# Kernel optimization log

Hardware: AMD Instinct MI355X
Metric: run time of the kernel (lower is better)

## Reference

```python
import jax, jax.numpy as jnp
import numpy as np

B, S, D, F, E, K = 4, 4096, 1024, 2048, 8, 2


def setup_inputs() -> dict:
    key = jax.random.key(0)
    ks = jax.random.split(key, 5)
    s = lambda n: 1.0 / np.sqrt(n).astype(np.float32)
    return {
        "hidden_states": jax.random.normal(ks[0], (B, S, D), jnp.float32),
        "router_w": jax.random.normal(ks[1], (E, D), jnp.float32) * s(D),
        "w_gate": jax.random.normal(ks[2], (E, F, D), jnp.float32) * s(D),
        "w_up": jax.random.normal(ks[3], (E, F, D), jnp.float32) * s(D),
        "w_down": jax.random.normal(ks[4], (E, D, F), jnp.float32) * s(F),
    }


def reference(hidden_states, router_w, w_gate, w_up, w_down):
    b, s, d = hidden_states.shape
    e = router_w.shape[0]
    x = hidden_states.reshape(-1, d)  # [T, D], T = B*S

    # --- router: softmax over expert logits, top-k, renormalize (norm_topk_prob) ---
    logits = x @ router_w.T                                   # [T, E]
    scores = jax.nn.softmax(logits.astype(jnp.float32), axis=-1)
    topk_w, topk_idx = jax.lax.top_k(scores, K)               # [T, K]
    topk_w = topk_w / jnp.sum(topk_w, axis=-1, keepdims=True)

    # dense per-(token, expert) combine weight: sum of topk weights routed to e
    cw = jnp.sum(jax.nn.one_hot(topk_idx, e, dtype=topk_w.dtype)
                 * topk_w[..., None], axis=1)                 # [T, E]
    cw = cw.astype(x.dtype)

    # --- experts: SwiGLU MLP per expert, weighted-combined; scan keeps memory low ---
    def per_expert(acc, wts):
        wg, wu, wd, cwe = wts                                  # [F,D],[F,D],[D,F],[T]
        h = jax.nn.silu(x @ wg.T) * (x @ wu.T)                 # [T, F]
        return acc + cwe[:, None] * (h @ wd.T), None

    out, _ = jax.lax.scan(per_expert, jnp.zeros_like(x),
                          (w_gate, w_up, w_down, cw.T))
    return out.reshape(b, s, d)
```

## Files before the change

### kernel.cpp

```cpp
#include <hip/hip_runtime.h>
#include <stdint.h>

#define T_TOK 16384
#define DDIM  1024
#define FDIM  2048
#define NEXP  8
#define MAX_SLOTS 33792
#define NMT (MAX_SLOTS / 128)

typedef __attribute__((ext_vector_type(8))) short bf16x8;
typedef __attribute__((ext_vector_type(4))) float f32x4;

typedef __attribute__((address_space(1))) void gvoid_t;
typedef __attribute__((address_space(3))) void lvoid_t;

#define META_CNT 0
#define META_CUR 256
#define META_OFF 512
#define META_MEXP 544

__device__ __forceinline__ void cp16(void* lds, const void* g) {
  __builtin_amdgcn_global_load_lds((gvoid_t*)g, (lvoid_t*)lds, 16, 0, 0);
}

__device__ __forceinline__ unsigned short f2bf(float f) {
  union { float f; unsigned int u; } v; v.f = f;
  unsigned int u = v.u;
  return (unsigned short)((u + 0x7fffu + ((u >> 16) & 1u)) >> 16);
}

__device__ __forceinline__ int xcd_remap(int bid, int nwg) {
  int xcd = bid & 7, i = bid >> 3;
  int q = nwg >> 3, r = nwg & 7;
  int base = (xcd < r) ? xcd * (q + 1) : r * (q + 1) + (xcd - r) * q;
  return base + i;
}

__global__ void router_kernel(const float* __restrict__ x, const float* __restrict__ rw,
                              int* __restrict__ tk_idx, float* __restrict__ tk_w,
                              unsigned short* __restrict__ xb) {
  const int wid = threadIdx.x >> 6;
  const int lane = threadIdx.x & 63;
  const int t = blockIdx.x * 4 + wid;
  const float4* xr = (const float4*)(x + (size_t)t * DDIM);
  float4 xv[4];
#pragma unroll
  for (int i = 0; i < 4; i++) xv[i] = xr[lane + 64 * i];
  ushort4* xbr = (ushort4*)(xb + (size_t)t * DDIM);
#pragma unroll
  for (int i = 0; i < 4; i++) {
    ushort4 o;
    o.x = f2bf(xv[i].x); o.y = f2bf(xv[i].y); o.z = f2bf(xv[i].z); o.w = f2bf(xv[i].w);
    xbr[lane + 64 * i] = o;
  }
  float lg[NEXP];
#pragma unroll
  for (int e = 0; e < NEXP; e++) {
    const float4* we = (const float4*)(rw + e * DDIM);
    float s = 0.f;
#pragma unroll
    for (int i = 0; i < 4; i++) {
      float4 v = we[lane + 64 * i];
      s += xv[i].x * v.x + xv[i].y * v.y + xv[i].z * v.z + xv[i].w * v.w;
    }
#pragma unroll
    for (int m = 32; m > 0; m >>= 1) s += __shfl_xor(s, m, 64);
    lg[e] = s;
  }
  int i0 = 0; float m0 = lg[0];
#pragma unroll
  for (int e = 1; e < NEXP; e++) if (lg[e] > m0) { m0 = lg[e]; i0 = e; }
  int i1 = -1; float m1 = -3.0e38f;
#pragma unroll
  for (int e = 0; e < NEXP; e++) if (e != i0 && lg[e] > m1) { m1 = lg[e]; i1 = e; }
  if (lane == 0) {
    float ee = __expf(m1 - m0);
    float w0 = 1.f / (1.f + ee);
    tk_idx[2 * t] = i0; tk_idx[2 * t + 1] = i1;
    tk_w[2 * t] = w0;  tk_w[2 * t + 1] = ee / (1.f + ee);
  }
}

__global__ void hist_kernel(const int* __restrict__ tk_idx, int* __restrict__ meta) {
  int* counts_p = meta + META_CNT;
  int t = blockIdx.x * 256 + threadIdx.x;
  int w = threadIdx.x >> 6, lane = threadIdx.x & 63;
  int e0 = tk_idx[2 * t], e1 = tk_idx[2 * t + 1];
  __shared__ int cnt[4][NEXP];
#pragma unroll
  for (int e = 0; e < NEXP; e++) {
    unsigned long long m0 = __ballot(e0 == e), m1 = __ballot(e1 == e);
    if (lane == 0) cnt[w][e] = __popcll(m0) + __popcll(m1);
  }
  __syncthreads();
  if (threadIdx.x < NEXP) {
    int e = threadIdx.x;
    atomicAdd(&counts_p[e * 32], cnt[0][e] + cnt[1][e] + cnt[2][e] + cnt[3][e]);
  }
}

__global__ void scan_kernel(int* __restrict__ meta) {
  int* counts_p = meta + META_CNT;
  int* offp     = meta + META_OFF;
  int* mexp     = meta + META_MEXP;
  __shared__ int soff[NEXP + 1];
  if (threadIdx.x == 0) {
    int acc = 0;
    for (int e = 0; e < NEXP; e++) {
      offp[e] = acc; soff[e] = acc;
      acc += (counts_p[e * 32] + 127) & ~127;
    }
    offp[NEXP] = acc; soff[NEXP] = acc;
  }
  __syncthreads();
  for (int m = threadIdx.x; m < NMT; m += blockDim.x) {
    int s = m * 128;
    int e = -1;
#pragma unroll
    for (int q = 0; q < NEXP; q++)
      if (s >= soff[q] && s < soff[q + 1]) { e = q; break; }
    mexp[m] = e;
  }
}

__global__ void scatter_kernel(const int* __restrict__ tk_idx, const float* __restrict__ tk_w,
                               int* __restrict__ meta,
                               int* __restrict__ slot_token, float* __restrict__ slot_w) {
  const int* offp = meta + META_OFF;
  int* cursors_p  = meta + META_CUR;
  int t = blockIdx.x * 256 + threadIdx.x;
  int w = threadIdx.x >> 6, lane = threadIdx.x & 63;
  int e0 = tk_idx[2 * t], e1 = tk_idx[2 * t + 1];
  unsigned long long lmask = (1ull << lane) - 1ull;
  __shared__ int cnt[4][NEXP], woff[4][NEXP], base[NEXP];
  int r0 = 0, r1 = 0;
#pragma unroll
  for (int e = 0; e < NEXP; e++) {
    unsigned long long m0 = __ballot(e0 == e), m1 = __ballot(e1 == e);
    int c0 = __popcll(m0);
    if (lane == 0) cnt[w][e] = c0 + __popcll(m1);
    if (e0 == e) r0 = __popcll(m0 & lmask);
    if (e1 == e) r1 = c0 + __popcll(m1 & lmask);
  }
  __syncthreads();
  if (threadIdx.x < NEXP) {
    int e = threadIdx.x, acc = 0;
#pragma unroll
    for (int ww = 0; ww < 4; ww++) { woff[ww][e] = acc; acc += cnt[ww][e]; }
    base[e] = atomicAdd(&cursors_p[e * 32], acc);
  }
  __syncthreads();
  int p0 = offp[e0] + base[e0] + woff[w][e0] + r0;
  int p1 = offp[e1] + base[e1] + woff[w][e1] + r1;
  slot_token[p0] = t; slot_w[p0] = tk_w[2 * t];
  slot_token[p1] = t; slot_w[p1] = tk_w[2 * t + 1];
}

#define W4EACH (1 << 22)
__global__ void cvt3_kernel(const float* __restrict__ wg, const float* __restrict__ wu,
                            const float* __restrict__ wd,
                            unsigned short* __restrict__ wgb, unsigned short* __restrict__ wub,
                            unsigned short* __restrict__ wdb) {
  int i = blockIdx.x * blockDim.x + threadIdx.x;
  int stride = gridDim.x * blockDim.x;
  for (; i < 3 * W4EACH; i += stride) {
    int which = i >> 22, j = i & (W4EACH - 1);
    const float4* s = (const float4*)(which == 0 ? wg : which == 1 ? wu : wd);
    ushort4* d = (ushort4*)(which == 0 ? wgb : which == 1 ? wub : wdb);
    float4 v = s[j];
    ushort4 o;
    o.x = f2bf(v.x); o.y = f2bf(v.y); o.z = f2bf(v.z); o.w = f2bf(v.w);
    d[j] = o;
  }
}

__global__ __launch_bounds__(256)
void gemm1_kernel(const unsigned short* __restrict__ xb,
                  const unsigned short* __restrict__ wgb,
                  const unsigned short* __restrict__ wub,
                  const int* __restrict__ meta,
                  const int* __restrict__ slot_token,
                  unsigned short* __restrict__ h, int m0) {
  const int wgid = xcd_remap((int)blockIdx.x, (int)gridDim.x);
  const int gm = m0 + (wgid >> 5);
  const int e = meta[META_MEXP + gm];
  if (e < 0) return;
  const int n0 = (wgid & 31) * 64;

  __shared__ alignas(16) unsigned short As[128 * 64];
  __shared__ alignas(16) unsigned short Bgs[64 * 64];
  __shared__ alignas(16) unsigned short Bus[64 * 64];

  const int tid = threadIdx.x;
  const int wid = tid >> 6;
  const int lane = tid & 63;
  const int wr = wid >> 1, wc = wid & 1;

  const unsigned int slog = (unsigned int)(((lane & 7) ^ (lane >> 3)) << 4);
  const char* const xbB = (const char*)xb;
  const char* const wgB = (const char*)wgb + ((size_t)e * FDIM + n0) * (DDIM * 2);
  const char* const wuB = (const char*)wub + ((size_t)e * FDIM + n0) * (DDIM * 2);

  const char* asrc[4]; unsigned int aldc[4];
#pragma unroll
  for (int q = 0; q < 4; q++) {
    int chunk = q * 4 + wid;
    int row = chunk * 8 + (lane >> 3);
    int tok = slot_token[gm * 128 + row];
    tok = tok < 0 ? 0 : tok;
    asrc[q] = xbB + (size_t)tok * (DDIM * 2) + slog;
    aldc[q] = chunk * 1024;
  }
  const char* bgsrc[2]; const char* busrc[2]; unsigned int bldc[2];
#pragma unroll
  for (int q = 0; q < 2; q++) {
    int chunk = q * 4 + wid;
    int row = chunk * 8 + (lane >> 3);
    bgsrc[q] = wgB + (size_t)row * (DDIM * 2) + slog;
    busrc[q] = wuB + (size_t)row * (DDIM * 2) + slog;
    bldc[q] = chunk * 1024;
  }

  const int lr = lane & 15, lk = lane >> 4;
  const unsigned int fsw = (unsigned int)((lane & 7) << 4);
  unsigned int aoff[4][2], boff[2][2];
#pragma unroll
  for (int mf = 0; mf < 4; mf++)
#pragma unroll
    for (int kc = 0; kc < 2; kc++) {
      unsigned int lg = (unsigned int)(kc * 64 + lk * 16);
      aoff[mf][kc] = (unsigned int)(wr * 64 + mf * 16 + lr) * 128 + (lg ^ fsw);
    }
#pragma unroll
  for (int nf = 0; nf < 2; nf++)
#pragma unroll
    for (int kc = 0; kc < 2; kc++) {
      unsigned int lg = (unsigned int)(kc * 64 + lk * 16);
      boff[nf][kc] = (unsigned int)(wc * 32 + nf * 16 + lr) * 128 + (lg ^ fsw);
    }

  f32x4 accg[4][2] = {};
  f32x4 accu[4][2] = {};
  const char* asb = (const char*)As;
  const char* bgsb = (const char*)Bgs;
  const char* busb = (const char*)Bus;

  for (int kt = 0; kt < DDIM / 64; kt++) {
    const int koff = kt * 128;
#pragma unroll
    for (int q = 0; q < 2; q++) {
      cp16((char*)Bgs + bldc[q], bgsrc[q] + koff);
      cp16((char*)Bus + bldc[q], busrc[q] + koff);
    }
#pragma unroll
    for (int q = 0; q < 4; q++) cp16((char*)As + aldc[q], asrc[q] + koff);
    __syncthreads();
#pragma unroll
    for (int kc = 0; kc < 2; kc++) {
      bf16x8 af[4], bgf[2], buf2[2];
#pragma unroll
      for (int mf = 0; mf < 4; mf++) af[mf] = *(const bf16x8*)(asb + aoff[mf][kc]);
#pragma unroll
      for (int nf = 0; nf < 2; nf++) {
        bgf[nf] = *(const bf16x8*)(bgsb + boff[nf][kc]);
        buf2[nf] = *(const bf16x8*)(busb + boff[nf][kc]);
      }
#pragma unroll
      for (int mf = 0; mf < 4; mf++)
#pragma unroll
        for (int nf = 0; nf < 2; nf++) {
          accg[mf][nf] = __builtin_amdgcn_mfma_f32_16x16x32_bf16(af[mf], bgf[nf], accg[mf][nf], 0, 0, 0);
          accu[mf][nf] = __builtin_amdgcn_mfma_f32_16x16x32_bf16(af[mf], buf2[nf], accu[mf][nf], 0, 0, 0);
        }
    }
    __syncthreads();
  }

  unsigned short* hB = h + (size_t)(gm - m0) * 128 * FDIM;
#pragma unroll
  for (int mf = 0; mf < 4; mf++)
#pragma unroll
    for (int nf = 0; nf < 2; nf++) {
      f32x4 g = accg[mf][nf], u = accu[mf][nf];
#pragma unroll
      for (int j = 0; j < 4; j++) {
        float gv = g[j];
        float hv = (gv / (1.f + __expf(-gv))) * u[j];
        int row = wr * 64 + mf * 16 + lk * 4 + j;
        int col = n0 + wc * 32 + nf * 16 + lr;
        hB[(size_t)row * FDIM + col] = f2bf(hv);
      }
    }
}

__global__ __launch_bounds__(256)
void gemm2_kernel(const unsigned short* __restrict__ h,
                  const unsigned short* __restrict__ wdb,
                  const int* __restrict__ meta,
                  const int* __restrict__ slot_token,
                  const float* __restrict__ slot_w,
                  float* __restrict__ out, int m0) {
  const int wgid = xcd_remap((int)blockIdx.x, (int)gridDim.x);
  const int gm = m0 + (wgid >> 3);
  const int e = meta[META_MEXP + gm];
  if (e < 0) return;
  const int n0 = (wgid & 7) * 128;

  __shared__ alignas(16) unsigned short As[128 * 64];
  __shared__ alignas(16) unsigned short Bs[128 * 64];

  const int tid = threadIdx.x;
  const int wid = tid >> 6;
  const int lane = tid & 63;
  const int wr = wid >> 1, wc = wid & 1;

  const unsigned int slog = (unsigned int)(((lane & 7) ^ (lane >> 3)) << 4);
  const char* const hB = (const char*)h + (size_t)(gm - m0) * 128 * (FDIM * 2);
  const char* const wdB = (const char*)wdb + ((size_t)e * DDIM + n0) * (FDIM * 2);

  const char* asrc[4]; const char* bsrc[4]; unsigned int ldc[4];
#pragma unroll
  for (int q = 0; q < 4; q++) {
    int chunk = q * 4 + wid;
    int row = chunk * 8 + (lane >> 3);
    asrc[q] = hB + (size_t)row * (FDIM * 2) + slog;
    bsrc[q] = wdB + (size_t)row * (FDIM * 2) + slog;
    ldc[q] = chunk * 1024;
  }

  const int lr = lane & 15, lk = lane >> 4;
  const unsigned int fsw = (unsigned int)((lane & 7) << 4);
  unsigned int aoff[4][2], boff[4][2];
#pragma unroll
  for (int f = 0; f < 4; f++)
#pragma unroll
    for (int kc = 0; kc < 2; kc++) {
      unsigned int lg = (unsigned int)(kc * 64 + lk * 16);
      aoff[f][kc] = (unsigned int)(wr * 64 + f * 16 + lr) * 128 + (lg ^ fsw);
      boff[f][kc] = (unsigned int)(wc * 64 + f * 16 + lr) * 128 + (lg ^ fsw);
    }

  f32x4 acc[4][4] = {};
  const char* asb = (const char*)As;
  const char* bsb = (const char*)Bs;

  for (int kt = 0; kt < FDIM / 64; kt++) {
    const int koff = kt * 128;
#pragma unroll
    for (int q = 0; q < 4; q++) {
      cp16((char*)As + ldc[q], asrc[q] + koff);
      cp16((char*)Bs + ldc[q], bsrc[q] + koff);
    }
    __syncthreads();
#pragma unroll
    for (int kc = 0; kc < 2; kc++) {
      bf16x8 af[4], bff[4];
#pragma unroll
      for (int mf = 0; mf < 4; mf++) af[mf] = *(const bf16x8*)(asb + aoff[mf][kc]);
#pragma unroll
      for (int nf = 0; nf < 4; nf++) bff[nf] = *(const bf16x8*)(bsb + boff[nf][kc]);
#pragma unroll
      for (int mf = 0; mf < 4; mf++)
#pragma unroll
        for (int nf = 0; nf < 4; nf++)
          acc[mf][nf] = __builtin_amdgcn_mfma_f32_16x16x32_bf16(af[mf], bff[nf], acc[mf][nf], 0, 0, 0);
    }
    __syncthreads();
  }

#pragma unroll
  for (int mf = 0; mf < 4; mf++)
#pragma unroll
    for (int j = 0; j < 4; j++) {
      int slot = gm * 128 + wr * 64 + mf * 16 + lk * 4 + j;
      int tok = slot_token[slot];
      if (tok < 0) continue;
      float w = slot_w[slot];
      float* orow = out + (size_t)tok * DDIM + n0 + wc * 64 + lr;
#pragma unroll
      for (int nf = 0; nf < 4; nf++)
        atomicAdd(orow + nf * 16, w * acc[mf][nf][j]);
    }
}

static constexpr size_t WB       = (size_t)NEXP * FDIM * DDIM * 2;
static constexpr size_t OFF_WG   = 0;
static constexpr size_t OFF_WU   = OFF_WG + WB;
static constexpr size_t OFF_WD   = OFF_WU + WB;
static constexpr size_t OFF_XB   = OFF_WD + WB;
static constexpr size_t XBB      = (size_t)T_TOK * DDIM * 2;
static constexpr size_t OFF_ST   = OFF_XB + XBB;
static constexpr size_t OFF_SW   = OFF_ST + (size_t)MAX_SLOTS * 4;
static constexpr size_t OFF_TI   = OFF_SW + (size_t)MAX_SLOTS * 4;
static constexpr size_t OFF_TW   = OFF_TI + (size_t)T_TOK * 2 * 4;
static constexpr size_t OFF_META = OFF_TW + (size_t)T_TOK * 2 * 4;
static constexpr size_t OFF_H    = OFF_ST + 1048576;
static constexpr size_t MT_BYTES = (size_t)128 * FDIM * 2;

extern "C" void kernel_launch(void* const* d_in, const int* in_sizes, int n_in,
                              void* d_out, int out_size, void* d_ws, size_t ws_size,
                              hipStream_t stream) {
  const float* x  = (const float*)d_in[0];
  const float* rw = (const float*)d_in[1];
  const float* wg = (const float*)d_in[2];
  const float* wu = (const float*)d_in[3];
  const float* wd = (const float*)d_in[4];
  float* out = (float*)d_out;

  char* ws = (char*)d_ws;
  unsigned short* wgb = (unsigned short*)(ws + OFF_WG);
  unsigned short* wub = (unsigned short*)(ws + OFF_WU);
  unsigned short* wdb = (unsigned short*)(ws + OFF_WD);
  unsigned short* xb  = (unsigned short*)(ws + OFF_XB);
  unsigned short* h   = (unsigned short*)(ws + OFF_H);
  int*   slot_token = (int*)(ws + OFF_ST);
  float* slot_w     = (float*)(ws + OFF_SW);
  int*   tk_idx     = (int*)(ws + OFF_TI);
  float* tk_w       = (float*)(ws + OFF_TW);
  int*   meta       = (int*)(ws + OFF_META);

  size_t avail = ws_size > OFF_H ? ws_size - OFF_H : 0;
  int wmt = (int)(avail / MT_BYTES);
  if (wmt > NMT) wmt = NMT;
  if (wmt < 8) wmt = 8;

  (void)hipMemsetAsync(out, 0, (size_t)out_size * sizeof(float), stream);
  (void)hipMemsetAsync(meta, 0, 2048, stream);
  (void)hipMemsetAsync(slot_token, 0xFF, (size_t)MAX_SLOTS * 4, stream);

  cvt3_kernel<<<4096, 256, 0, stream>>>(wg, wu, wd, wgb, wub, wdb);
  router_kernel<<<T_TOK / 4, 256, 0, stream>>>(x, rw, tk_idx, tk_w, xb);
  hist_kernel<<<T_TOK / 256, 256, 0, stream>>>(tk_idx, meta);
  scan_kernel<<<1, 256, 0, stream>>>(meta);
  scatter_kernel<<<T_TOK / 256, 256, 0, stream>>>(tk_idx, tk_w, meta, slot_token, slot_w);

  for (int m0 = 0; m0 < NMT; m0 += wmt) {
    int mc = (NMT - m0 < wmt) ? (NMT - m0) : wmt;
    gemm1_kernel<<<mc * 32, 256, 0, stream>>>(xb, wgb, wub, meta, slot_token, h, m0);
    gemm2_kernel<<<mc * 8, 256, 0, stream>>>(h, wdb, meta, slot_token, slot_w, out, m0);
  }
}
```

Measured before the change: 759.1 us.

## Pre-gather routed tokens into contiguous bf16 buffer and enlarge gemm1 N tile

Replaces the router's dense bf16 copy of x with a gather kernel that writes routed tokens into a slot-ordered contiguous bf16 buffer, so gemm1 reads A rows contiguously instead of indirecting through slot_token. Gemm1's N tile doubles from 64 to 128, giving each wave a 4x4 fragment grid so each A fragment is reused across more MFMAs, and the gate and up MFMAs are split into separate phases. It also drops the XCD-aware block remap in favour of a plain 2D grid. The costs are an extra gather pass over about 33K slots, higher register and LDS pressure that may lower occupancy, and possibly worse L2 locality across XCDs.

```diff
diff --git a/kernel.cpp b/kernel.cpp
--- a/kernel.cpp
+++ b/kernel.cpp
@@ -37,8 +37,7 @@
 }
 
 __global__ void router_kernel(const float* __restrict__ x, const float* __restrict__ rw,
-                              int* __restrict__ tk_idx, float* __restrict__ tk_w,
-                              unsigned short* __restrict__ xb) {
+                              int* __restrict__ tk_idx, float* __restrict__ tk_w) {
   const int wid = threadIdx.x >> 6;
   const int lane = threadIdx.x & 63;
   const int t = blockIdx.x * 4 + wid;
@@ -46,13 +45,6 @@
   float4 xv[4];
 #pragma unroll
   for (int i = 0; i < 4; i++) xv[i] = xr[lane + 64 * i];
-  ushort4* xbr = (ushort4*)(xb + (size_t)t * DDIM);
-#pragma unroll
-  for (int i = 0; i < 4; i++) {
-    ushort4 o;
-    o.x = f2bf(xv[i].x); o.y = f2bf(xv[i].y); o.z = f2bf(xv[i].z); o.w = f2bf(xv[i].w);
-    xbr[lane + 64 * i] = o;
-  }
   float lg[NEXP];
 #pragma unroll
   for (int e = 0; e < NEXP; e++) {
@@ -174,22 +166,35 @@
   }
 }
 
+__global__ void gather_kernel(const float* __restrict__ x, const int* __restrict__ slot_token,
+                              unsigned short* __restrict__ xg) {
+  int slot = blockIdx.x;
+  int t = slot_token[slot];
+  int c = threadIdx.x * 4;
+  ushort4 o;
+  if (t >= 0) {
+    float4 v = *(const float4*)(x + (size_t)t * DDIM + c);
+    o.x = f2bf(v.x); o.y = f2bf(v.y); o.z = f2bf(v.z); o.w = f2bf(v.w);
+  } else {
+    o.x = 0; o.y = 0; o.z = 0; o.w = 0;
+  }
+  *(ushort4*)(xg + (size_t)slot * DDIM + c) = o;
+}
+
 __global__ __launch_bounds__(256)
-void gemm1_kernel(const unsigned short* __restrict__ xb,
+void gemm1_kernel(const unsigned short* __restrict__ xg,
                   const unsigned short* __restrict__ wgb,
                   const unsigned short* __restrict__ wub,
                   const int* __restrict__ meta,
-                  const int* __restrict__ slot_token,
                   unsigned short* __restrict__ h, int m0) {
-  const int wgid = xcd_remap((int)blockIdx.x, (int)gridDim.x);
-  const int gm = m0 + (wgid >> 5);
+  const int gm = m0 + blockIdx.y;
   const int e = meta[META_MEXP + gm];
   if (e < 0) return;
-  const int n0 = (wgid & 31) * 64;
+  const int n0 = blockIdx.x * 128;
 
   __shared__ alignas(16) unsigned short As[128 * 64];
-  __shared__ alignas(16) unsigned short Bgs[64 * 64];
-  __shared__ alignas(16) unsigned short Bus[64 * 64];
+  __shared__ alignas(16) unsigned short Bgs[128 * 64];
+  __shared__ alignas(16) unsigned short Bus[128 * 64];
 
   const int tid = threadIdx.x;
   const int wid = tid >> 6;
@@ -197,50 +202,35 @@
   const int wr = wid >> 1, wc = wid & 1;
 
   const unsigned int slog = (unsigned int)(((lane & 7) ^ (lane >> 3)) << 4);
-  const char* const xbB = (const char*)xb;
+  const char* const xgB = (const char*)xg;
   const char* const wgB = (const char*)wgb + ((size_t)e * FDIM + n0) * (DDIM * 2);
   const char* const wuB = (const char*)wub + ((size_t)e * FDIM + n0) * (DDIM * 2);
 
-  const char* asrc[4]; unsigned int aldc[4];
+  const char* asrc[4]; const char* bgsrc[4]; const char* busrc[4]; unsigned int ldc[4];
 #pragma unroll
   for (int q = 0; q < 4; q++) {
     int chunk = q * 4 + wid;
     int row = chunk * 8 + (lane >> 3);
-    int tok = slot_token[gm * 128 + row];
-    tok = tok < 0 ? 0 : tok;
-    asrc[q] = xbB + (size_t)tok * (DDIM * 2) + slog;
-    aldc[q] = chunk * 1024;
-  }
-  const char* bgsrc[2]; const char* busrc[2]; unsigned int bldc[2];
-#pragma unroll
-  for (int q = 0; q < 2; q++) {
-    int chunk = q * 4 + wid;
-    int row = chunk * 8 + (lane >> 3);
+    asrc[q]  = xgB + (size_t)(gm * 128 + row) * (DDIM * 2) + slog;
     bgsrc[q] = wgB + (size_t)row * (DDIM * 2) + slog;
     busrc[q] = wuB + (size_t)row * (DDIM * 2) + slog;
-    bldc[q] = chunk * 1024;
+    ldc[q] = chunk * 1024;
   }
 
   const int lr = lane & 15, lk = lane >> 4;
   const unsigned int fsw = (unsigned int)((lane & 7) << 4);
-  unsigned int aoff[4][2], boff[2][2];
-#pragma unroll
-  for (int mf = 0; mf < 4; mf++)
+  unsigned int aoff[4][2], boff[4][2];
+#pragma unroll
+  for (int f = 0; f < 4; f++)
 #pragma unroll
     for (int kc = 0; kc < 2; kc++) {
       unsigned int lg = (unsigned int)(kc * 64 + lk * 16);
-      aoff[mf][kc] = (unsigned int)(wr * 64 + mf * 16 + lr) * 128 + (lg ^ fsw);
-    }
-#pragma unroll
-  for (int nf = 0; nf < 2; nf++)
-#pragma unroll
-    for (int kc = 0; kc < 2; kc++) {
-      unsigned int lg = (unsigned int)(kc * 64 + lk * 16);
-      boff[nf][kc] = (unsigned int)(wc * 32 + nf * 16 + lr) * 128 + (lg ^ fsw);
-    }
-
-  f32x4 accg[4][2] = {};
-  f32x4 accu[4][2] = {};
+      aoff[f][kc] = (unsigned int)(wr * 64 + f * 16 + lr) * 128 + (lg ^ fsw);
+      boff[f][kc] = (unsigned int)(wc * 64 + f * 16 + lr) * 128 + (lg ^ fsw);
+    }
+
+  f32x4 accg[4][4] = {};
+  f32x4 accu[4][4] = {};
   const char* asb = (const char*)As;
   const char* bgsb = (const char*)Bgs;
   const char* busb = (const char*)Bus;
@@ -248,30 +238,31 @@
   for (int kt = 0; kt < DDIM / 64; kt++) {
     const int koff = kt * 128;
 #pragma unroll
-    for (int q = 0; q < 2; q++) {
-      cp16((char*)Bgs + bldc[q], bgsrc[q] + koff);
-      cp16((char*)Bus + bldc[q], busrc[q] + koff);
-    }
-#pragma unroll
-    for (int q = 0; q < 4; q++) cp16((char*)As + aldc[q], asrc[q] + koff);
+    for (int q = 0; q < 4; q++) {
+      cp16((char*)As + ldc[q], asrc[q] + koff);
+      cp16((char*)Bgs + ldc[q], bgsrc[q] + koff);
+      cp16((char*)Bus + ldc[q], busrc[q] + koff);
+    }
     __syncthreads();
 #pragma unroll
     for (int kc = 0; kc < 2; kc++) {
-      bf16x8 af[4], bgf[2], buf2[2];
+      bf16x8 af[4], bgf[4], buf2[4];
 #pragma unroll
       for (int mf = 0; mf < 4; mf++) af[mf] = *(const bf16x8*)(asb + aoff[mf][kc]);
 #pragma unroll
-      for (int nf = 0; nf < 2; nf++) {
-        bgf[nf] = *(const bf16x8*)(bgsb + boff[nf][kc]);
-        buf2[nf] = *(const bf16x8*)(busb + boff[nf][kc]);
-      }
+      for (int nf = 0; nf < 4; nf++) bgf[nf] = *(const bf16x8*)(bgsb + boff[nf][kc]);
 #pragma unroll
       for (int mf = 0; mf < 4; mf++)
 #pragma unroll
-        for (int nf = 0; nf < 2; nf++) {
+        for (int nf = 0; nf < 4; nf++)
           accg[mf][nf] = __builtin_amdgcn_mfma_f32_16x16x32_bf16(af[mf], bgf[nf], accg[mf][nf], 0, 0, 0);
+#pragma unroll
+      for (int nf = 0; nf < 4; nf++) buf2[nf] = *(const bf16x8*)(busb + boff[nf][kc]);
+#pragma unroll
+      for (int mf = 0; mf < 4; mf++)
+#pragma unroll
+        for (int nf = 0; nf < 4; nf++)
           accu[mf][nf] = __builtin_amdgcn_mfma_f32_16x16x32_bf16(af[mf], buf2[nf], accu[mf][nf], 0, 0, 0);
-        }
     }
     __syncthreads();
   }
@@ -280,14 +271,14 @@
 #pragma unroll
   for (int mf = 0; mf < 4; mf++)
 #pragma unroll
-    for (int nf = 0; nf < 2; nf++) {
+    for (int nf = 0; nf < 4; nf++) {
       f32x4 g = accg[mf][nf], u = accu[mf][nf];
 #pragma unroll
       for (int j = 0; j < 4; j++) {
         float gv = g[j];
         float hv = (gv / (1.f + __expf(-gv))) * u[j];
         int row = wr * 64 + mf * 16 + lk * 4 + j;
-        int col = n0 + wc * 32 + nf * 16 + lr;
+        int col = n0 + wc * 64 + nf * 16 + lr;
         hB[(size_t)row * FDIM + col] = f2bf(hv);
       }
     }
@@ -387,9 +378,9 @@
 static constexpr size_t OFF_WG   = 0;
 static constexpr size_t OFF_WU   = OFF_WG + WB;
 static constexpr size_t OFF_WD   = OFF_WU + WB;
-static constexpr size_t OFF_XB   = OFF_WD + WB;
-static constexpr size_t XBB      = (size_t)T_TOK * DDIM * 2;
-static constexpr size_t OFF_ST   = OFF_XB + XBB;
+static constexpr size_t OFF_XG   = OFF_WD + WB;
+static constexpr size_t XGB      = (size_t)MAX_SLOTS * DDIM * 2;
+static constexpr size_t OFF_ST   = OFF_XG + XGB;
 static constexpr size_t OFF_SW   = OFF_ST + (size_t)MAX_SLOTS * 4;
 static constexpr size_t OFF_TI   = OFF_SW + (size_t)MAX_SLOTS * 4;
 static constexpr size_t OFF_TW   = OFF_TI + (size_t)T_TOK * 2 * 4;
@@ -411,7 +402,7 @@
   unsigned short* wgb = (unsigned short*)(ws + OFF_WG);
   unsigned short* wub = (unsigned short*)(ws + OFF_WU);
   unsigned short* wdb = (unsigned short*)(ws + OFF_WD);
-  unsigned short* xb  = (unsigned short*)(ws + OFF_XB);
+  unsigned short* xg  = (unsigned short*)(ws + OFF_XG);
   unsigned short* h   = (unsigned short*)(ws + OFF_H);
   int*   slot_token = (int*)(ws + OFF_ST);
   float* slot_w     = (float*)(ws + OFF_SW);
@@ -429,14 +420,15 @@
   (void)hipMemsetAsync(slot_token, 0xFF, (size_t)MAX_SLOTS * 4, stream);
 
   cvt3_kernel<<<4096, 256, 0, stream>>>(wg, wu, wd, wgb, wub, wdb);
-  router_kernel<<<T_TOK / 4, 256, 0, stream>>>(x, rw, tk_idx, tk_w, xb);
+  router_kernel<<<T_TOK / 4, 256, 0, stream>>>(x, rw, tk_idx, tk_w);
   hist_kernel<<<T_TOK / 256, 256, 0, stream>>>(tk_idx, meta);
   scan_kernel<<<1, 256, 0, stream>>>(meta);
   scatter_kernel<<<T_TOK / 256, 256, 0, stream>>>(tk_idx, tk_w, meta, slot_token, slot_w);
+  gather_kernel<<<MAX_SLOTS, 256, 0, stream>>>(x, slot_token, xg);
 
   for (int m0 = 0; m0 < NMT; m0 += wmt) {
     int mc = (NMT - m0 < wmt) ? (NMT - m0) : wmt;
-    gemm1_kernel<<<mc * 32, 256, 0, stream>>>(xb, wgb, wub, meta, slot_token, h, m0);
+    gemm1_kernel<<<dim3(FDIM / 128, mc), 256, 0, stream>>>(xg, wgb, wub, meta, h, m0);
     gemm2_kernel<<<mc * 8, 256, 0, stream>>>(h, wdb, meta, slot_token, slot_w, out, m0);
   }
 }
```

After: 1.025 ms. +35.0%, slower.

## Pre-gather routed token rows into contiguous buffer before gate/up GEMM

Applied to the files above, without the earlier changes.

Adds a gather kernel that copies each slot's bf16 token row into a dense per-slot buffer, so gemm1 loads A tiles from contiguous rows instead of indirecting through slot_token. It also drops the XCD-aware block remapping in favour of a 2D grid. The cost is an extra pass that writes about 69MB and a larger workspace, which shifts the start of h and shrinks the number of m-tiles per chunk. Losing the XCD remap may also reduce L2 reuse of the weights.

```diff
diff --git a/kernel.cpp b/kernel.cpp
--- a/kernel.cpp
+++ b/kernel.cpp
@@ -174,18 +174,28 @@
   }
 }
 
+__global__ void gather_kernel(const unsigned short* __restrict__ xb,
+                              const int* __restrict__ slot_token,
+                              unsigned short* __restrict__ xg) {
+  int slot = blockIdx.x;
+  int t = slot_token[slot];
+  int c = threadIdx.x * 4;
+  ushort4 o;
+  if (t >= 0) o = *(const ushort4*)(xb + (size_t)t * DDIM + c);
+  else { o.x = 0; o.y = 0; o.z = 0; o.w = 0; }
+  *(ushort4*)(xg + (size_t)slot * DDIM + c) = o;
+}
+
 __global__ __launch_bounds__(256)
-void gemm1_kernel(const unsigned short* __restrict__ xb,
+void gemm1_kernel(const unsigned short* __restrict__ xg,
                   const unsigned short* __restrict__ wgb,
                   const unsigned short* __restrict__ wub,
                   const int* __restrict__ meta,
-                  const int* __restrict__ slot_token,
                   unsigned short* __restrict__ h, int m0) {
-  const int wgid = xcd_remap((int)blockIdx.x, (int)gridDim.x);
-  const int gm = m0 + (wgid >> 5);
+  const int gm = m0 + blockIdx.y;
   const int e = meta[META_MEXP + gm];
   if (e < 0) return;
-  const int n0 = (wgid & 31) * 64;
+  const int n0 = blockIdx.x * 64;
 
   __shared__ alignas(16) unsigned short As[128 * 64];
   __shared__ alignas(16) unsigned short Bgs[64 * 64];
@@ -197,7 +207,7 @@
   const int wr = wid >> 1, wc = wid & 1;
 
   const unsigned int slog = (unsigned int)(((lane & 7) ^ (lane >> 3)) << 4);
-  const char* const xbB = (const char*)xb;
+  const char* const xgB = (const char*)xg;
   const char* const wgB = (const char*)wgb + ((size_t)e * FDIM + n0) * (DDIM * 2);
   const char* const wuB = (const char*)wub + ((size_t)e * FDIM + n0) * (DDIM * 2);
 
@@ -206,9 +216,7 @@
   for (int q = 0; q < 4; q++) {
     int chunk = q * 4 + wid;
     int row = chunk * 8 + (lane >> 3);
-    int tok = slot_token[gm * 128 + row];
-    tok = tok < 0 ? 0 : tok;
-    asrc[q] = xbB + (size_t)tok * (DDIM * 2) + slog;
+    asrc[q] = xgB + (size_t)(gm * 128 + row) * (DDIM * 2) + slog;
     aldc[q] = chunk * 1024;
   }
   const char* bgsrc[2]; const char* busrc[2]; unsigned int bldc[2];
@@ -389,7 +397,9 @@
 static constexpr size_t OFF_WD   = OFF_WU + WB;
 static constexpr size_t OFF_XB   = OFF_WD + WB;
 static constexpr size_t XBB      = (size_t)T_TOK * DDIM * 2;
-static constexpr size_t OFF_ST   = OFF_XB + XBB;
+static constexpr size_t OFF_XG   = OFF_XB + XBB;
+static constexpr size_t XGB      = (size_t)MAX_SLOTS * DDIM * 2;
+static constexpr size_t OFF_ST   = OFF_XG + XGB;
 static constexpr size_t OFF_SW   = OFF_ST + (size_t)MAX_SLOTS * 4;
 static constexpr size_t OFF_TI   = OFF_SW + (size_t)MAX_SLOTS * 4;
 static constexpr size_t OFF_TW   = OFF_TI + (size_t)T_TOK * 2 * 4;
@@ -412,6 +422,7 @@
   unsigned short* wub = (unsigned short*)(ws + OFF_WU);
   unsigned short* wdb = (unsigned short*)(ws + OFF_WD);
   unsigned short* xb  = (unsigned short*)(ws + OFF_XB);
+  unsigned short* xg  = (unsigned short*)(ws + OFF_XG);
   unsigned short* h   = (unsigned short*)(ws + OFF_H);
   int*   slot_token = (int*)(ws + OFF_ST);
   float* slot_w     = (float*)(ws + OFF_SW);
@@ -433,10 +444,11 @@
   hist_kernel<<<T_TOK / 256, 256, 0, stream>>>(tk_idx, meta);
   scan_kernel<<<1, 256, 0, stream>>>(meta);
   scatter_kernel<<<T_TOK / 256, 256, 0, stream>>>(tk_idx, tk_w, meta, slot_token, slot_w);
+  gather_kernel<<<MAX_SLOTS, 256, 0, stream>>>(xb, slot_token, xg);
 
   for (int m0 = 0; m0 < NMT; m0 += wmt) {
     int mc = (NMT - m0 < wmt) ? (NMT - m0) : wmt;
-    gemm1_kernel<<<mc * 32, 256, 0, stream>>>(xb, wgb, wub, meta, slot_token, h, m0);
+    gemm1_kernel<<<dim3(FDIM / 64, mc), 256, 0, stream>>>(xg, wgb, wub, meta, h, m0);
     gemm2_kernel<<<mc * 8, 256, 0, stream>>>(h, wdb, meta, slot_token, slot_w, out, m0);
   }
 }
```

Result: no change. 769.2 us (+1.3%).

## Fuse expert histogram into router and drop XCD remap in gemm1

Applied to the files above, without the earlier changes.

Expert counts are now accumulated inside the router kernel with shared-memory atomics and one global atomic per expert per block, which removes the separate histogram kernel launch and its re-read of top-k indices. The gemm1 launch switches to a 2D grid (N tiles by M tiles) and drops the XCD-aware block remap. Blocks sharing an M tile are now spread across XCDs, which changes L2 reuse of the token rows. The router also gains a block barrier and many more global atomics (4096 blocks × 8).

```diff
diff --git a/kernel.cpp b/kernel.cpp
--- a/kernel.cpp
+++ b/kernel.cpp
@@ -38,10 +38,12 @@
 
 __global__ void router_kernel(const float* __restrict__ x, const float* __restrict__ rw,
                               int* __restrict__ tk_idx, float* __restrict__ tk_w,
-                              unsigned short* __restrict__ xb) {
+                              unsigned short* __restrict__ xb, int* __restrict__ meta) {
   const int wid = threadIdx.x >> 6;
   const int lane = threadIdx.x & 63;
   const int t = blockIdx.x * 4 + wid;
+  __shared__ int cnt[NEXP];
+  if (threadIdx.x < NEXP) cnt[threadIdx.x] = 0;
   const float4* xr = (const float4*)(x + (size_t)t * DDIM);
   float4 xv[4];
 #pragma unroll
@@ -73,30 +75,18 @@
   int i1 = -1; float m1 = -3.0e38f;
 #pragma unroll
   for (int e = 0; e < NEXP; e++) if (e != i0 && lg[e] > m1) { m1 = lg[e]; i1 = e; }
+  __syncthreads();
   if (lane == 0) {
     float ee = __expf(m1 - m0);
     float w0 = 1.f / (1.f + ee);
     tk_idx[2 * t] = i0; tk_idx[2 * t + 1] = i1;
     tk_w[2 * t] = w0;  tk_w[2 * t + 1] = ee / (1.f + ee);
-  }
-}
-
-__global__ void hist_kernel(const int* __restrict__ tk_idx, int* __restrict__ meta) {
-  int* counts_p = meta + META_CNT;
-  int t = blockIdx.x * 256 + threadIdx.x;
-  int w = threadIdx.x >> 6, lane = threadIdx.x & 63;
-  int e0 = tk_idx[2 * t], e1 = tk_idx[2 * t + 1];
-  __shared__ int cnt[4][NEXP];
-#pragma unroll
-  for (int e = 0; e < NEXP; e++) {
-    unsigned long long m0 = __ballot(e0 == e), m1 = __ballot(e1 == e);
-    if (lane == 0) cnt[w][e] = __popcll(m0) + __popcll(m1);
+    atomicAdd(&cnt[i0], 1);
+    atomicAdd(&cnt[i1], 1);
   }
   __syncthreads();
-  if (threadIdx.x < NEXP) {
-    int e = threadIdx.x;
-    atomicAdd(&counts_p[e * 32], cnt[0][e] + cnt[1][e] + cnt[2][e] + cnt[3][e]);
-  }
+  if (threadIdx.x < NEXP)
+    atomicAdd(&meta[META_CNT + threadIdx.x * 32], cnt[threadIdx.x]);
 }
 
 __global__ void scan_kernel(int* __restrict__ meta) {
@@ -181,11 +171,10 @@
                   const int* __restrict__ meta,
                   const int* __restrict__ slot_token,
                   unsigned short* __restrict__ h, int m0) {
-  const int wgid = xcd_remap((int)blockIdx.x, (int)gridDim.x);
-  const int gm = m0 + (wgid >> 5);
+  const int gm = m0 + blockIdx.y;
   const int e = meta[META_MEXP + gm];
   if (e < 0) return;
-  const int n0 = (wgid & 31) * 64;
+  const int n0 = blockIdx.x * 64;
 
   __shared__ alignas(16) unsigned short As[128 * 64];
   __shared__ alignas(16) unsigned short Bgs[64 * 64];
@@ -429,14 +418,13 @@
   (void)hipMemsetAsync(slot_token, 0xFF, (size_t)MAX_SLOTS * 4, stream);
 
   cvt3_kernel<<<4096, 256, 0, stream>>>(wg, wu, wd, wgb, wub, wdb);
-  router_kernel<<<T_TOK / 4, 256, 0, stream>>>(x, rw, tk_idx, tk_w, xb);
-  hist_kernel<<<T_TOK / 256, 256, 0, stream>>>(tk_idx, meta);
+  router_kernel<<<T_TOK / 4, 256, 0, stream>>>(x, rw, tk_idx, tk_w, xb, meta);
   scan_kernel<<<1, 256, 0, stream>>>(meta);
   scatter_kernel<<<T_TOK / 256, 256, 0, stream>>>(tk_idx, tk_w, meta, slot_token, slot_w);
 
   for (int m0 = 0; m0 < NMT; m0 += wmt) {
     int mc = (NMT - m0 < wmt) ? (NMT - m0) : wmt;
-    gemm1_kernel<<<mc * 32, 256, 0, stream>>>(xb, wgb, wub, meta, slot_token, h, m0);
+    gemm1_kernel<<<dim3(FDIM / 64, mc), 256, 0, stream>>>(xb, wgb, wub, meta, slot_token, h, m0);
     gemm2_kernel<<<mc * 8, 256, 0, stream>>>(h, wdb, meta, slot_token, slot_w, out, m0);
   }
 }
```

Result: no change. 768.1 us (+1.2%).
